# Kernel optimization log

Measured on AMD Instinct MI355X. Metric: run time of the kernel, lower is better.

Reference implementation:

```python
import jax, jax.numpy as jnp
import numpy as np
from jax import lax

B, T_PAST, T_FUT, F_IN, F_OUT, H = 512, 128, 48, 64, 16, 512


def setup_inputs() -> dict:
    key = jax.random.key(0)
    ks = jax.random.split(key, 12)
    s = jnp.float32(0.05)
    p = lambda k, shape: jax.random.normal(k, shape, jnp.float32) * s
    return {
        "inp": jax.random.normal(ks[0], (B, T_PAST, F_IN), jnp.float32),
        "target_seq": jax.random.normal(ks[1], (B, T_FUT, F_OUT), jnp.float32),
        "enc1_Wk": p(ks[2], (F_IN, 4 * H)), "enc1_Wr": p(ks[3], (H, 4 * H)), "enc1_b": jnp.zeros((4 * H,), jnp.float32),
        "enc2_Wk": p(ks[4], (H, 4 * H)), "enc2_Wr": p(ks[5], (H, 4 * H)), "enc2_b": jnp.zeros((4 * H,), jnp.float32),
        "dec1_Wk": p(ks[6], (F_OUT, 4 * H)), "dec1_Wr": p(ks[7], (H, 4 * H)), "dec1_b": jnp.zeros((4 * H,), jnp.float32),
        "dec2_Wk": p(ks[8], (H, 4 * H)), "dec2_Wr": p(ks[9], (H, 4 * H)), "dec2_b": jnp.zeros((4 * H,), jnp.float32),
        "fc_W": p(ks[10], (H, F_OUT)), "fc_b": jnp.zeros((F_OUT,), jnp.float32),
    }


def _gates(z, c_prev):
    # Keras gate order: i, f, g(cell), o
    i, f, g, o = jnp.split(z, 4, axis=-1)
    c = jax.nn.sigmoid(f) * c_prev + jax.nn.sigmoid(i) * jnp.tanh(g)
    h = jax.nn.sigmoid(o) * jnp.tanh(c)
    return h, c


def _lstm_layer(xs, h0, c0, Wk, Wr, b):
    # xs: (B, T, D) -> (hs (B,T,H), hT, cT)
    xz = jnp.einsum("btd,dg->btg", xs, Wk) + b  # input projection precomputed
    def step(carry, xz_t):
        h, c = carry
        h2, c2 = _gates(xz_t + h @ Wr, c)
        return (h2, c2), h2
    (hT, cT), hs = lax.scan(step, (h0, c0), jnp.swapaxes(xz, 0, 1))
    return jnp.swapaxes(hs, 0, 1), hT, cT


def reference(inp, target_seq,
              enc1_Wk, enc1_Wr, enc1_b, enc2_Wk, enc2_Wr, enc2_b,
              dec1_Wk, dec1_Wr, dec1_b, dec2_Wk, dec2_Wr, dec2_b,
              fc_W, fc_b):
    b = inp.shape[0]
    z = jnp.zeros((b, H), inp.dtype)
    # Encoder: layer2 initial state = layer1 final state (as in source)
    h1s, h1, c1 = _lstm_layer(inp, z, z, enc1_Wk, enc1_Wr, enc1_b)
    _, h2, c2 = _lstm_layer(h1s, h1, c1, enc2_Wk, enc2_Wr, enc2_b)
    # Decoder: every future step restarts from (h2, c2) with teacher-forced
    # inputs -> steps are independent, compute all in parallel.
    z1 = (jnp.einsum("btf,fg->btg", target_seq, dec1_Wk)
          + (h2 @ dec1_Wr)[:, None, :] + dec1_b)          # (B, Tf, 4H)
    h1d, c1d = _gates(z1, c2[:, None, :])
    # layer2: input = h1d, initial state = (h1d, c1d) (chained per source)
    z2 = jnp.einsum("bth,hg->btg", h1d, dec2_Wk + dec2_Wr) + dec2_b
    h2d, _ = _gates(z2, c1d)
    return jnp.einsum("bth,hf->btf", h2d, fc_W) + fc_b    # (B, Tf, F_OUT)
```

## Files before the change

kernel.cpp:

```cpp
#include <hip/hip_runtime.h>


typedef _Float16 f16;
typedef _Float16 h8 __attribute__((ext_vector_type(8)));
typedef _Float16 h4 __attribute__((ext_vector_type(4)));
typedef _Float16 h2v __attribute__((ext_vector_type(2)));
typedef float f32x4 __attribute__((ext_vector_type(4)));
typedef float f32x2 __attribute__((ext_vector_type(2)));
typedef unsigned long long ull;

#define DEV static __device__ __forceinline__

constexpr int NB   = 512;
constexpr int TP   = 128;
constexpr int TFU  = 48;
constexpr int FIN  = 64;
constexpr int FOUT = 16;
constexpr int HS   = 512;
constexpr int G4   = 2048;

DEV float sigf(float x) { return 1.0f / (1.0f + __expf(-x)); }
DEV float tanh_(float x) { float e = __expf(2.0f * x); return 1.0f - 2.0f / (e + 1.0f); }

DEV void issue_ld(h8& d, const f16* p) {
  asm volatile("global_load_dwordx4 %0, %1, off" : "=v"(d) : "v"(p));
}
DEV void issue_ldc(h8& d, const f16* p) {
  asm volatile("global_load_dwordx4 %0, %1, off sc0 sc1" : "=v"(d) : "v"(p));
}
#define ASM_VM0    asm volatile("s_waitcnt vmcnt(0)" ::: "memory")
#define ASM_VMC(N) asm volatile("s_waitcnt vmcnt(" #N ")" ::: "memory")
#define SBAR       __builtin_amdgcn_sched_barrier(0)

DEV void st_coh_h2(f16* p, h2v v) {
  union { h2v h; unsigned u; } c;
  c.h = v;
  __hip_atomic_store((unsigned*)p, c.u, __ATOMIC_RELAXED, __HIP_MEMORY_SCOPE_AGENT);
}

DEV unsigned xcc_id() {
  unsigned x;
  asm("s_getreg_b32 %0, hwreg(HW_REG_XCC_ID)" : "=s"(x));
  return x & 7;
}

DEV int ic2zc(int ic) { return ((ic >> 4) & 3) * 512 + ((ic >> 6) << 4) + (ic & 15); }

__global__ void k_conv(const float* __restrict__ a, const float* __restrict__ b,
                       f16* __restrict__ a16, f16* __restrict__ b16) {
  const size_t NA = (size_t)NB * TP * FIN;
  const size_t NBT = (size_t)NB * TFU * FOUT;
  for (size_t i = (size_t)blockIdx.x * blockDim.x + threadIdx.x; i < NA + NBT;
       i += (size_t)gridDim.x * blockDim.x) {
    if (i < NA) a16[i] = (f16)a[i];
    else        b16[i - NA] = (f16)b[i - NA];
  }
}

__global__ void k_bias(const float* __restrict__ b1, const float* __restrict__ b2,
                       const float* __restrict__ b3, const float* __restrict__ b4,
                       float* __restrict__ o1, float* __restrict__ o2,
                       float* __restrict__ o3, float* __restrict__ o4) {
  int ic = blockIdx.x * blockDim.x + threadIdx.x;
  if (ic < G4) {
    int zc = ic2zc(ic);
    o1[ic] = b1[zc]; o2[ic] = b2[zc]; o3[ic] = b3[zc]; o4[ic] = b4[zc];
  }
}

__global__ void k_pack(const float* __restrict__ A, const float* __restrict__ Bs,
                       int split, int NKC, int mode, f16* __restrict__ dst) {
  int i = blockIdx.x * blockDim.x + threadIdx.x;
  int total = 128 * NKC * 64;
  if (i >= total) return;
  int lane = i & 63, rem = i >> 6;
  int kc = rem % NKC, nt = rem / NKC;
  int zc = ic2zc(nt * 16 + (lane & 15));
  int k0 = kc * 32 + ((lane >> 4) << 3);
  h8 v;
#pragma unroll
  for (int j = 0; j < 8; j++) {
    int k = k0 + j;
    float x;
    if (mode == 2) x = A[(size_t)k * G4 + zc] + Bs[(size_t)k * G4 + zc];
    else x = (k < split) ? A[(size_t)k * G4 + zc] : Bs[(size_t)(k - split) * G4 + zc];
    v[j] = (f16)x;
  }
  *(h8*)(dst + (size_t)i * 8) = v;
}

__global__ void k_pack_dk16(const float* __restrict__ W, f16* __restrict__ dst) {
  int i = blockIdx.x * blockDim.x + threadIdx.x;
  if (i >= 128 * 64) return;
  int lane = i & 63, nt = i >> 6;
  int zc = ic2zc(nt * 16 + (lane & 15));
  h4 v;
#pragma unroll
  for (int j = 0; j < 4; j++) v[j] = (f16)W[(size_t)(((lane >> 4) << 2) + j) * G4 + zc];
  *(h4*)(dst + (size_t)i * 4) = v;
}

__global__ void k_pack_fc(const float* __restrict__ W, f16* __restrict__ dst) {
  int i = blockIdx.x * blockDim.x + threadIdx.x;
  if (i >= 32 * 64) return;
  int lane = i & 63, q = i >> 6;
  h4 v;
#pragma unroll
  for (int j = 0; j < 4; j++) {
    int k = q * 16 + ((lane >> 4) << 2) + j;
    v[j] = (f16)W[(size_t)k * FOUT + (lane & 15)];
  }
  *(h4*)(dst + (size_t)i * 4) = v;
}

template <int L, bool HIST>
__global__ __launch_bounds__(512, 2) void k_enc(
    const f16* __restrict__ wfrag, const float* __restrict__ biasI,
    f16* __restrict__ h1s, f16* __restrict__ h2r, f16* __restrict__ h2s,
    float* __restrict__ cT, const float* __restrict__ cInit,
    const f16* __restrict__ inp16, unsigned int* __restrict__ cnt,
    int* __restrict__ roster) {
  constexpr int XKC = (L == 1) ? 2 : 16;
  constexpr int XKH = XKC / 2;
  constexpr int NKC = XKC + 16;
  constexpr size_t SLOT = (size_t)NB * HS;
  constexpr bool PLAIN_H = (L == 1) || HIST;

  extern __shared__ __align__(16) char smem[];
  f16* Bl = (f16*)smem;
  float* zl = (float*)(smem + (size_t)NKC * 4096);
  __shared__ int s_gc[2];

  const int tid = threadIdx.x, lane = tid & 63, wid = tid >> 6;
  const int wr4 = wid & 3, ks = wid >> 2;

  if (tid == 0) {
    unsigned x = xcc_id();
    int slot = atomicAdd(&roster[x], 1) & 31;
    s_gc[0] = (int)x; s_gc[1] = slot;
  }
  __syncthreads();
  const int g = s_gc[0], c = s_gc[1];
  const int b0 = g * 64;
  const int l15 = lane & 15, lk = (lane >> 4) << 3;
  const int trow = tid >> 3, tcol = (tid & 7) << 1;

  const int kc0 = ((c >> 1) + 1) & 15;

  {
    const uint4* src = (const uint4*)wfrag + (size_t)c * NKC * 256;
    uint4* dst = (uint4*)smem;
    for (int i = tid; i < NKC * 256; i += 512) dst[i] = src[i];
  }

  float bs[4][2];
#pragma unroll
  for (int ga = 0; ga < 4; ga++) {
    f32x2 bv = *(const f32x2*)(biasI + 64 * c + 16 * ga + tcol);
    bs[ga][0] = bv[0]; bs[ga][1] = bv[1];
  }

  float cst[2];
  if (L == 1) {
    cst[0] = cst[1] = 0.0f;
  } else {
    f32x2 cv = *(const f32x2*)(cInit + (size_t)(b0 + trow) * HS + 16 * c + tcol);
    cst[0] = cv[0]; cst[1] = cv[1];
  }

  const int arow = b0 + 16 * wr4 + l15;

  const f16* bbase[4];
#pragma unroll
  for (int n = 0; n < 4; n++) bbase[n] = Bl + ((size_t)n * NKC * 64 + lane) * 8;

  const size_t aoff = ((size_t)(lk >> 4) * 512 + arow) * 16 + (lk & 8);

  unsigned int* cbase = cnt + (size_t)g * TP * 16;

  __syncthreads();

  for (int t = 0; t < TP; t++) {
    h8 ax[XKH];
    if (L == 1) {
      const f16* xb = inp16 + ((size_t)arow * TP + t) * FIN + lk + ks * 32;
      issue_ld(ax[0], xb);
    } else {
      const f16* xp = h1s + (size_t)(t + 1) * SLOT + aoff + (size_t)ks * XKH * 16384;
#pragma unroll
      for (int kc = 0; kc < XKH; kc++) {
        issue_ld(ax[kc], xp);
        xp += 16384;
      }
    }
    ASM_VM0; SBAR;

    f32x4 acc[4] = {};
#pragma unroll
    for (int kc = 0; kc < XKH; kc++) {
      int kg = ks * XKH + kc;
#pragma unroll
      for (int n = 0; n < 4; n++) {
        h8 bb = *(const h8*)(bbase[n] + (size_t)kg * 512);
        acc[n] = __builtin_amdgcn_mfma_f32_16x16x32_f16(ax[kc], bb, acc[n], 0, 0, 0);
      }
    }

    if (t > 0) {
      const unsigned int* cp = cbase + (size_t)(t - 1) * 16;
      while (__hip_atomic_load(cp, __ATOMIC_RELAXED, __HIP_MEMORY_SCOPE_AGENT) < 32u)
        __builtin_amdgcn_s_sleep(1);
      SBAR;
    }

    const f16* hb;
    if (L == 1) hb = h1s + (size_t)t * SLOT;
    else if (HIST) hb = (t == 0) ? (h1s + (size_t)TP * SLOT) : (h2s + (size_t)(t - 1) * SLOT);
    else hb = (t == 0) ? (h1s + (size_t)TP * SLOT) : (h2r + (size_t)((t - 1) & 1) * SLOT);
    const f16* hpb = hb + aoff;

    h8 hA[4], hB[4];
#define LD_H(D, P) { if constexpr (PLAIN_H) issue_ld(D, P); else issue_ldc(D, P); }
#define HB_ISSUE4(R, P)                                                        \
  {                                                                            \
    _Pragma("unroll") for (int j = 0; j < 4; j++) {                            \
      int kk = (kc0 + 8 * ks + (P) + j) & 15;                                  \
      const f16* q = hpb + (size_t)kk * 16384;                                 \
      LD_H(R[j], q)                                                            \
    }                                                                          \
  }
#define HB_MFMA4(R, P)                                                         \
  {                                                                            \
    _Pragma("unroll") for (int j = 0; j < 4; j++) {                            \
      int kk = (kc0 + 8 * ks + (P) + j) & 15;                                  \
      _Pragma("unroll") for (int n = 0; n < 4; n++) {                          \
        h8 bb = *(const h8*)(bbase[n] + (size_t)(XKC + kk) * 512);             \
        acc[n] = __builtin_amdgcn_mfma_f32_16x16x32_f16(R[j], bb, acc[n], 0, 0, 0); \
      }                                                                        \
    }                                                                          \
  }

    HB_ISSUE4(hA, 0)
    HB_ISSUE4(hB, 4)
    ASM_VMC(4); SBAR;
    HB_MFMA4(hA, 0)
    ASM_VMC(0); SBAR;
    HB_MFMA4(hB, 4)
#undef HB_ISSUE4
#undef HB_MFMA4
#undef LD_H

    {
      int zr = 16 * wr4 + ((lane >> 4) << 2);
      if (ks == 0) {
#pragma unroll
        for (int n = 0; n < 4; n++) {
          int zc_ = 16 * n + l15;
#pragma unroll
          for (int r = 0; r < 4; r++) zl[(size_t)(zr + r) * 68 + zc_] = acc[n][r];
        }
      }
      __syncthreads();
      if (ks == 1) {
#pragma unroll
        for (int n = 0; n < 4; n++) {
          int zc_ = 16 * n + l15;
#pragma unroll
          for (int r = 0; r < 4; r++) {
            float* p = &zl[(size_t)(zr + r) * 68 + zc_];
            *p += acc[n][r];
          }
        }
      }
      __syncthreads();
    }

    h2v hv;
    {
      const float* zrow = zl + (size_t)trow * 68 + tcol;
      f32x2 z0 = *(const f32x2*)(zrow + 0);
      f32x2 z1 = *(const f32x2*)(zrow + 16);
      f32x2 z2 = *(const f32x2*)(zrow + 32);
      f32x2 z3 = *(const f32x2*)(zrow + 48);
#pragma unroll
      for (int jj = 0; jj < 2; jj++) {
        float zi = z0[jj] + bs[0][jj];
        float zf = z1[jj] + bs[1][jj];
        float zg = z2[jj] + bs[2][jj];
        float zo = z3[jj] + bs[3][jj];
        float ci = sigf(zf) * cst[jj] + sigf(zi) * tanh_(zg);
        cst[jj] = ci;
        hv[jj] = (f16)(sigf(zo) * tanh_(ci));
      }
    }
    {
      f16* hsl;
      if (L == 1) hsl = h1s + (size_t)(t + 1) * SLOT;
      else if (HIST) hsl = h2s + (size_t)t * SLOT;
      else hsl = h2r + (size_t)(t & 1) * SLOT;
      f16* hp = hsl + ((size_t)c * 512 + b0 + trow) * 16 + tcol;
      if constexpr (PLAIN_H) *(h2v*)hp = hv;
      else st_coh_h2(hp, hv);
    }
    if (t == TP - 1) {
      f32x2 cp;
      cp[0] = cst[0]; cp[1] = cst[1];
      *(f32x2*)(cT + (size_t)(b0 + trow) * HS + 16 * c + tcol) = cp;
    }

    ASM_VM0;
    __syncthreads();
    if (tid == 0)
      __hip_atomic_fetch_add(cbase + (size_t)t * 16, 1u, __ATOMIC_RELAXED,
                             __HIP_MEMORY_SCOPE_AGENT);
  }
}

__global__ __launch_bounds__(256) void k_d1(const f16* __restrict__ h2T,
                                            const f16* __restrict__ wF,
                                            const float* __restrict__ bI,
                                            float* __restrict__ u) {
  const int tid = threadIdx.x, lane = tid & 63, wid = tid >> 6;
  const int wr = wid & 1, wc = wid >> 1;
  const int r0 = (blockIdx.x >> 4) * 32, ic0 = (blockIdx.x & 15) * 128;
  const int l15 = lane & 15, lk = (lane >> 4) << 3;
  const int arow = r0 + 16 * wr + l15;
  const f16* abase = h2T + ((size_t)(lk >> 4) * 512 + arow) * 16 + (lk & 8);
  const int nt0 = (ic0 >> 4) + 4 * wc;
  f32x4 acc[4] = {};
#pragma unroll
  for (int kc = 0; kc < 16; kc++) {
    h8 a = *(const h8*)(abase + (size_t)kc * 16384);
#pragma unroll
    for (int n = 0; n < 4; n++) {
      h8 b = *(const h8*)(wF + ((size_t)(nt0 + n) * 16 + kc) * 512 + (size_t)lane * 8);
      acc[n] = __builtin_amdgcn_mfma_f32_16x16x32_f16(a, b, acc[n], 0, 0, 0);
    }
  }
#pragma unroll
  for (int n = 0; n < 4; n++)
#pragma unroll
    for (int r = 0; r < 4; r++) {
      int row = r0 + 16 * wr + ((lane >> 4) << 2) + r;
      int ic = ic0 + 64 * wc + 16 * n + l15;
      u[(size_t)row * G4 + ic] = acc[n][r] + bI[ic];
    }
}

__global__ __launch_bounds__(256, 1) void k_d2(
    const f16* __restrict__ tg16, const f16* __restrict__ wk16F,
    const float* __restrict__ u, const float* __restrict__ c2T,
    const f16* __restrict__ w2F, const float* __restrict__ b2I,
    const f16* __restrict__ fcF, const float* __restrict__ fcb,
    float* __restrict__ out) {
  extern __shared__ __align__(16) char smem[];
  constexpr size_t H1OFF = 0;
  constexpr size_t C1OFF = 65536;
  constexpr size_t H2OFF = 131072;
  constexpr size_t RDOFF = 143360;

  const int tid = threadIdx.x, lane = tid & 63, wid = tid >> 6;
  const int l15 = lane & 15;
  const int r0 = blockIdx.x * 64;

  {
    const int wr = wid & 1, wc = wid >> 1;
    h4 a[2];
#pragma unroll
    for (int m = 0; m < 2; m++)
      a[m] = *(const h4*)(tg16 + (size_t)(r0 + 32 * wr + 16 * m + l15) * FOUT +
                          ((lane >> 4) << 2));
#pragma unroll 1
    for (int hc = 0; hc < 8; hc++) {
      f32x4 acc[2][8] = {};
#pragma unroll
      for (int n = 0; n < 8; n++) {
        int ntg = 16 * hc + 8 * wc + n;
        h4 b = *(const h4*)(wk16F + ((size_t)ntg * 64 + lane) * 4);
        acc[0][n] = __builtin_amdgcn_mfma_f32_16x16x16f16(a[0], b, acc[0][n], 0, 0, 0);
        acc[1][n] = __builtin_amdgcn_mfma_f32_16x16x16f16(a[1], b, acc[1][n], 0, 0, 0);
      }
#pragma unroll
      for (int m = 0; m < 2; m++)
#pragma unroll
        for (int s = 0; s < 2; s++) {
          int qq = 4 * hc + 2 * wc + s;
          int colh = 16 * qq + l15;
          int icb = 256 * hc + 128 * wc + 64 * s + l15;
#pragma unroll
          for (int r = 0; r < 4; r++) {
            int rl = 32 * wr + 16 * m + ((lane >> 4) << 2) + r;
            int grow = r0 + rl;
            int bidx = grow / 48;
            const float* ub = u + (size_t)bidx * G4;
            float zi = acc[m][4 * s + 0][r] + ub[icb];
            float zf = acc[m][4 * s + 1][r] + ub[icb + 16];
            float zg = acc[m][4 * s + 2][r] + ub[icb + 32];
            float zo = acc[m][4 * s + 3][r] + ub[icb + 48];
            float c2v = c2T[(size_t)bidx * HS + colh];
            float c1 = sigf(zf) * c2v + sigf(zi) * tanh_(zg);
            float h1 = sigf(zo) * tanh_(c1);
            size_t hb = (((size_t)rl * 1024) + (size_t)colh * 2) ^ (size_t)((rl & 7) << 4);
            *(f16*)(smem + H1OFF + hb) = (f16)h1;
            *(f16*)(smem + C1OFF + (size_t)rl * 1024 + (size_t)colh * 2) = (f16)c1;
          }
        }
    }
  }
  __syncthreads();

  {
    const int w = wid;
    f32x4 facc[4] = {};
#pragma unroll 1
    for (int sc = 0; sc < 8; sc++) {
      f32x4 acc[4][4] = {};
#pragma unroll
      for (int kc = 0; kc < 16; kc++) {
        h8 a[4];
#pragma unroll
        for (int mt = 0; mt < 4; mt++) {
          int rl = 16 * mt + l15;
          size_t ab = (((size_t)rl * 1024) + (size_t)(kc * 32 + ((lane >> 4) << 3)) * 2) ^
                      (size_t)((rl & 7) << 4);
          a[mt] = *(const h8*)(smem + H1OFF + ab);
        }
#pragma unroll
        for (int n = 0; n < 4; n++) {
          int nt = 32 * w + 4 * sc + n;
          h8 b = *(const h8*)(w2F + ((size_t)nt * 16 + kc) * 512 + (size_t)lane * 8);
#pragma unroll
          for (int mt = 0; mt < 4; mt++)
            acc[mt][n] = __builtin_amdgcn_mfma_f32_16x16x32_f16(a[mt], b, acc[mt][n], 0, 0, 0);
        }
      }
      int qq = 8 * w + sc;
#pragma unroll
      for (int mt = 0; mt < 4; mt++)
#pragma unroll
        for (int r = 0; r < 4; r++) {
          int rl = 16 * mt + ((lane >> 4) << 2) + r;
          int colh = 16 * qq + l15;
          int ic = 512 * w + 64 * sc + l15;
          float zi = acc[mt][0][r] + b2I[ic];
          float zf = acc[mt][1][r] + b2I[ic + 16];
          float zg = acc[mt][2][r] + b2I[ic + 32];
          float zo = acc[mt][3][r] + b2I[ic + 48];
          float c1v = (float)*(const f16*)(smem + C1OFF + (size_t)rl * 1024 + (size_t)colh * 2);
          float cn = sigf(zf) * c1v + sigf(zi) * tanh_(zg);
          float h2v_ = sigf(zo) * tanh_(cn);
          *(f16*)(smem + H2OFF + (size_t)w * 3072 + (size_t)rl * 48 + (size_t)l15 * 2) = (f16)h2v_;
        }
#pragma unroll
      for (int mt = 0; mt < 4; mt++) {
        h4 aa = *(const h4*)(smem + H2OFF + (size_t)w * 3072 + (size_t)(16 * mt + l15) * 48 +
                             ((lane >> 4) << 3));
        h4 bb = *(const h4*)(fcF + ((size_t)qq * 64 + lane) * 4);
        facc[mt] = __builtin_amdgcn_mfma_f32_16x16x16f16(aa, bb, facc[mt], 0, 0, 0);
      }
    }
#pragma unroll
    for (int mt = 0; mt < 4; mt++)
#pragma unroll
      for (int r = 0; r < 4; r++) {
        int rl = 16 * mt + ((lane >> 4) << 2) + r;
        *(float*)(smem + RDOFF + ((size_t)w * 1152 + (size_t)rl * 18 + l15) * 4) = facc[mt][r];
      }
  }
  __syncthreads();

  {
    int rl = tid >> 2, c4 = (tid & 3) * 4;
    f32x4 o;
#pragma unroll
    for (int j = 0; j < 4; j++) {
      float s = 0.0f;
#pragma unroll
      for (int w = 0; w < 4; w++)
        s += *(const float*)(smem + RDOFF + ((size_t)w * 1152 + (size_t)rl * 18 + c4 + j) * 4);
      o[j] = s + fcb[c4 + j];
    }
    *(f32x4*)(out + (size_t)(r0 + rl) * FOUT + c4) = o;
  }
}

extern "C" void kernel_launch(void* const* d_in, const int* in_sizes, int n_in,
                              void* d_out, int out_size, void* d_ws, size_t ws_size,
                              hipStream_t stream) {
  const float* inp     = (const float*)d_in[0];
  const float* target  = (const float*)d_in[1];
  const float* e1Wk    = (const float*)d_in[2];
  const float* e1Wr    = (const float*)d_in[3];
  const float* e1b     = (const float*)d_in[4];
  const float* e2Wk    = (const float*)d_in[5];
  const float* e2Wr    = (const float*)d_in[6];
  const float* e2b     = (const float*)d_in[7];
  const float* d1Wk    = (const float*)d_in[8];
  const float* d1Wr    = (const float*)d_in[9];
  const float* d1b     = (const float*)d_in[10];
  const float* d2Wk    = (const float*)d_in[11];
  const float* d2Wr    = (const float*)d_in[12];
  const float* d2b     = (const float*)d_in[13];
  const float* fcW     = (const float*)d_in[14];
  const float* fcb     = (const float*)d_in[15];
  float* out = (float*)d_out;

  char* ws = (char*)d_ws;
  size_t off = 0;
  auto carve = [&](size_t bytes) { char* p = ws + off; off += bytes; return p; };
  f16*   inp16 = (f16*)carve((size_t)NB * TP * FIN * 2);
  f16*   tg16  = (f16*)carve((size_t)NB * TFU * FOUT * 2);
  f16*   h1s   = (f16*)carve((size_t)(TP + 1) * NB * HS * 2);
  f16*   h2r   = (f16*)carve((size_t)2 * NB * HS * 2);
  float* c1T   = (float*)carve((size_t)NB * HS * 4);
  float* c2T   = (float*)carve((size_t)NB * HS * 4);
  float* ubuf  = (float*)carve((size_t)NB * G4 * 4);
  f16*   Wc1F  = (f16*)carve((size_t)576 * G4 * 2);
  f16*   Wc2F  = (f16*)carve((size_t)1024 * G4 * 2);
  f16*   d1WrF = (f16*)carve((size_t)512 * G4 * 2);
  f16*   W2sF  = (f16*)carve((size_t)512 * G4 * 2);
  f16*   dk16F = (f16*)carve((size_t)16 * G4 * 2);
  f16*   fcWF  = (f16*)carve((size_t)512 * FOUT * 2);
  float* eB1I  = (float*)carve((size_t)G4 * 4);
  float* eB2I  = (float*)carve((size_t)G4 * 4);
  float* dB1I  = (float*)carve((size_t)G4 * 4);
  float* dB2I  = (float*)carve((size_t)G4 * 4);
  unsigned int* cnt1 = (unsigned int*)carve((size_t)8 * TP * 64);
  unsigned int* cnt2 = (unsigned int*)carve((size_t)8 * TP * 64);
  int*   roster = (int*)carve(256);
  const size_t H2S_BYTES = (size_t)TP * NB * HS * 2;
  bool hist = (ws_size >= off + H2S_BYTES);
  f16* h2s = hist ? (f16*)carve(H2S_BYTES) : nullptr;
  (void)n_in; (void)in_sizes; (void)out_size;

  constexpr int LDS_E1 = 18 * 4096 + 64 * 68 * 4;
  constexpr int LDS_E2 = 32 * 4096 + 64 * 68 * 4;
  constexpr int LDS_D2 = 143360 + 18432;
  {
    void (*p1)(const f16*, const float*, f16*, f16*, f16*, float*, const float*, const f16*,
               unsigned int*, int*) = k_enc<1, true>;
    void (*p2a)(const f16*, const float*, f16*, f16*, f16*, float*, const float*, const f16*,
                unsigned int*, int*) = k_enc<2, true>;
    void (*p2b)(const f16*, const float*, f16*, f16*, f16*, float*, const float*, const f16*,
                unsigned int*, int*) = k_enc<2, false>;
    hipFuncSetAttribute((const void*)p1, hipFuncAttributeMaxDynamicSharedMemorySize, LDS_E1);
    hipFuncSetAttribute((const void*)p2a, hipFuncAttributeMaxDynamicSharedMemorySize, LDS_E2);
    hipFuncSetAttribute((const void*)p2b, hipFuncAttributeMaxDynamicSharedMemorySize, LDS_E2);
    hipFuncSetAttribute((const void*)k_d2, hipFuncAttributeMaxDynamicSharedMemorySize, LDS_D2);
  }

  hipMemsetAsync(cnt1, 0, (size_t)2 * 8 * TP * 64 + 256, stream);
  hipMemsetAsync(h1s, 0, (size_t)NB * HS * 2, stream);

  k_conv<<<4096, 256, 0, stream>>>(inp, target, inp16, tg16);
  k_bias<<<8, 256, 0, stream>>>(e1b, e2b, d1b, d2b, eB1I, eB2I, dB1I, dB2I);
  k_pack<<<576, 256, 0, stream>>>(e1Wk, e1Wr, 64, 18, 1, Wc1F);
  k_pack<<<1024, 256, 0, stream>>>(e2Wk, e2Wr, 512, 32, 1, Wc2F);
  k_pack<<<512, 256, 0, stream>>>(d1Wr, d1Wr, 512, 16, 1, d1WrF);
  k_pack<<<512, 256, 0, stream>>>(d2Wk, d2Wr, 0, 16, 2, W2sF);
  k_pack_dk16<<<32, 256, 0, stream>>>(d1Wk, dk16F);
  k_pack_fc<<<8, 256, 0, stream>>>(fcW, fcWF);

  k_enc<1, true><<<256, 512, LDS_E1, stream>>>(Wc1F, eB1I, h1s, h2r, h2s, c1T, nullptr,
                                               inp16, cnt1, roster);
  int* roster2 = roster + 8;
  if (hist)
    k_enc<2, true><<<256, 512, LDS_E2, stream>>>(Wc2F, eB2I, h1s, h2r, h2s, c2T, c1T,
                                                 nullptr, cnt2, roster2);
  else
    k_enc<2, false><<<256, 512, LDS_E2, stream>>>(Wc2F, eB2I, h1s, h2r, h2s, c2T, c1T,
                                                  nullptr, cnt2, roster2);

  const f16* h2T = hist ? (h2s + (size_t)(TP - 1) * NB * HS) : (h2r + (size_t)1 * NB * HS);
  k_d1<<<256, 256, 0, stream>>>(h2T, d1WrF, dB1I, ubuf);
  k_d2<<<384, 256, LDS_D2, stream>>>(tg16, dk16F, ubuf, c2T, W2sF, dB2I, fcWF, fcb, out);
}
```

Measured before the change: 1.291 ms.

## Exchange half-accumulators between K-split waves and defer input MFMA past wait

The LDS reduction of the two K-split partial sums, which took two block barriers and a full z tile round-trip, becomes a single barrier exchange. Each wave writes only the half of its accumulator rows that its partner needs, then finishes gates for its own two rows straight from registers. The input-projection loads are issued before the spin-wait on the previous step's counter, and their MFMAs now run after the hidden-state loads are issued, overlapping the wait and load latency. The cost is narrower global stores of h and c (single f16 or float per lane instead of pairs), including 16-bit coherent atomic stores.

```diff
diff --git a/kernel.cpp b/kernel.cpp
--- a/kernel.cpp
+++ b/kernel.cpp
@@ -32,10 +32,10 @@
 #define ASM_VMC(N) asm volatile("s_waitcnt vmcnt(" #N ")" ::: "memory")
 #define SBAR       __builtin_amdgcn_sched_barrier(0)
 
-DEV void st_coh_h2(f16* p, h2v v) {
-  union { h2v h; unsigned u; } c;
+DEV void st_coh_h1(f16* p, f16 v) {
+  union { f16 h; unsigned short u; } c;
   c.h = v;
-  __hip_atomic_store((unsigned*)p, c.u, __ATOMIC_RELAXED, __HIP_MEMORY_SCOPE_AGENT);
+  __hip_atomic_store((unsigned short*)p, c.u, __ATOMIC_RELAXED, __HIP_MEMORY_SCOPE_AGENT);
 }
 
 DEV unsigned xcc_id() {
@@ -128,7 +128,7 @@
 
   extern __shared__ __align__(16) char smem[];
   f16* Bl = (f16*)smem;
-  float* zl = (float*)(smem + (size_t)NKC * 4096);
+  float* exl = (float*)(smem + (size_t)NKC * 4096);
   __shared__ int s_gc[2];
 
   const int tid = threadIdx.x, lane = tid & 63, wid = tid >> 6;
@@ -143,7 +143,6 @@
   const int g = s_gc[0], c = s_gc[1];
   const int b0 = g * 64;
   const int l15 = lane & 15, lk = (lane >> 4) << 3;
-  const int trow = tid >> 3, tcol = (tid & 7) << 1;
 
   const int kc0 = ((c >> 1) + 1) & 15;
 
@@ -153,19 +152,19 @@
     for (int i = tid; i < NKC * 256; i += 512) dst[i] = src[i];
   }
 
-  float bs[4][2];
-#pragma unroll
-  for (int ga = 0; ga < 4; ga++) {
-    f32x2 bv = *(const f32x2*)(biasI + 64 * c + 16 * ga + tcol);
-    bs[ga][0] = bv[0]; bs[ga][1] = bv[1];
-  }
+  float bv[4];
+#pragma unroll
+  for (int n = 0; n < 4; n++) bv[n] = biasI[64 * c + 16 * n + l15];
+
+  const int grow0 = b0 + 16 * wr4 + ((lane >> 4) << 2) + 2 * ks;
 
   float cst[2];
   if (L == 1) {
     cst[0] = cst[1] = 0.0f;
   } else {
-    f32x2 cv = *(const f32x2*)(cInit + (size_t)(b0 + trow) * HS + 16 * c + tcol);
-    cst[0] = cv[0]; cst[1] = cv[1];
+#pragma unroll
+    for (int j = 0; j < 2; j++)
+      cst[j] = cInit[(size_t)(grow0 + j) * HS + 16 * c + l15];
   }
 
   const int arow = b0 + 16 * wr4 + l15;
@@ -177,6 +176,9 @@
   const size_t aoff = ((size_t)(lk >> 4) * 512 + arow) * 16 + (lk & 8);
 
   unsigned int* cbase = cnt + (size_t)g * TP * 16;
+
+  const int myslot = wr4 * 2 + ks, pslot = wr4 * 2 + (ks ^ 1);
+  const int j2p = 2 * (ks ^ 1);
 
   __syncthreads();
 
@@ -193,24 +195,14 @@
         xp += 16384;
       }
     }
-    ASM_VM0; SBAR;
-
-    f32x4 acc[4] = {};
-#pragma unroll
-    for (int kc = 0; kc < XKH; kc++) {
-      int kg = ks * XKH + kc;
-#pragma unroll
-      for (int n = 0; n < 4; n++) {
-        h8 bb = *(const h8*)(bbase[n] + (size_t)kg * 512);
-        acc[n] = __builtin_amdgcn_mfma_f32_16x16x32_f16(ax[kc], bb, acc[n], 0, 0, 0);
-      }
-    }
 
     if (t > 0) {
       const unsigned int* cp = cbase + (size_t)(t - 1) * 16;
       while (__hip_atomic_load(cp, __ATOMIC_RELAXED, __HIP_MEMORY_SCOPE_AGENT) < 32u)
         __builtin_amdgcn_s_sleep(1);
       SBAR;
+    } else {
+      ASM_VM0; SBAR;
     }
 
     const f16* hb;
@@ -242,6 +234,19 @@
 
     HB_ISSUE4(hA, 0)
     HB_ISSUE4(hB, 4)
+
+    f32x4 acc[4] = {};
+
+#pragma unroll
+    for (int kc = 0; kc < XKH; kc++) {
+      int kg = ks * XKH + kc;
+#pragma unroll
+      for (int n = 0; n < 4; n++) {
+        h8 bb = *(const h8*)(bbase[n] + (size_t)kg * 512);
+        acc[n] = __builtin_amdgcn_mfma_f32_16x16x32_f16(ax[kc], bb, acc[n], 0, 0, 0);
+      }
+    }
+
     ASM_VMC(4); SBAR;
     HB_MFMA4(hA, 0)
     ASM_VMC(0); SBAR;
@@ -250,62 +255,40 @@
 #undef HB_MFMA4
 #undef LD_H
 
-    {
-      int zr = 16 * wr4 + ((lane >> 4) << 2);
-      if (ks == 0) {
-#pragma unroll
-        for (int n = 0; n < 4; n++) {
-          int zc_ = 16 * n + l15;
-#pragma unroll
-          for (int r = 0; r < 4; r++) zl[(size_t)(zr + r) * 68 + zc_] = acc[n][r];
-        }
-      }
-      __syncthreads();
-      if (ks == 1) {
-#pragma unroll
-        for (int n = 0; n < 4; n++) {
-          int zc_ = 16 * n + l15;
-#pragma unroll
-          for (int r = 0; r < 4; r++) {
-            float* p = &zl[(size_t)(zr + r) * 68 + zc_];
-            *p += acc[n][r];
-          }
-        }
-      }
-      __syncthreads();
-    }
-
-    h2v hv;
-    {
-      const float* zrow = zl + (size_t)trow * 68 + tcol;
-      f32x2 z0 = *(const f32x2*)(zrow + 0);
-      f32x2 z1 = *(const f32x2*)(zrow + 16);
-      f32x2 z2 = *(const f32x2*)(zrow + 32);
-      f32x2 z3 = *(const f32x2*)(zrow + 48);
-#pragma unroll
-      for (int jj = 0; jj < 2; jj++) {
-        float zi = z0[jj] + bs[0][jj];
-        float zf = z1[jj] + bs[1][jj];
-        float zg = z2[jj] + bs[2][jj];
-        float zo = z3[jj] + bs[3][jj];
-        float ci = sigf(zf) * cst[jj] + sigf(zi) * tanh_(zg);
-        cst[jj] = ci;
-        hv[jj] = (f16)(sigf(zo) * tanh_(ci));
-      }
+#pragma unroll
+    for (int n = 0; n < 4; n++)
+#pragma unroll
+      for (int j = 0; j < 2; j++)
+        exl[(size_t)myslot * 512 + (size_t)(n * 2 + j) * 64 + lane] = acc[n][j2p + j];
+    __syncthreads();
+
+    f16 hval[2];
+#pragma unroll
+    for (int j = 0; j < 2; j++) {
+      float zi = acc[0][2 * ks + j] + exl[(size_t)pslot * 512 + (size_t)(0 + j) * 64 + lane] + bv[0];
+      float zf = acc[1][2 * ks + j] + exl[(size_t)pslot * 512 + (size_t)(2 + j) * 64 + lane] + bv[1];
+      float zg = acc[2][2 * ks + j] + exl[(size_t)pslot * 512 + (size_t)(4 + j) * 64 + lane] + bv[2];
+      float zo = acc[3][2 * ks + j] + exl[(size_t)pslot * 512 + (size_t)(6 + j) * 64 + lane] + bv[3];
+      float ci = sigf(zf) * cst[j] + sigf(zi) * tanh_(zg);
+      cst[j] = ci;
+      hval[j] = (f16)(sigf(zo) * tanh_(ci));
     }
     {
       f16* hsl;
       if (L == 1) hsl = h1s + (size_t)(t + 1) * SLOT;
       else if (HIST) hsl = h2s + (size_t)t * SLOT;
       else hsl = h2r + (size_t)(t & 1) * SLOT;
-      f16* hp = hsl + ((size_t)c * 512 + b0 + trow) * 16 + tcol;
-      if constexpr (PLAIN_H) *(h2v*)hp = hv;
-      else st_coh_h2(hp, hv);
+#pragma unroll
+      for (int j = 0; j < 2; j++) {
+        f16* hp = hsl + ((size_t)c * 512 + grow0 + j) * 16 + l15;
+        if constexpr (PLAIN_H) *hp = hval[j];
+        else st_coh_h1(hp, hval[j]);
+      }
     }
     if (t == TP - 1) {
-      f32x2 cp;
-      cp[0] = cst[0]; cp[1] = cst[1];
-      *(f32x2*)(cT + (size_t)(b0 + trow) * HS + 16 * c + tcol) = cp;
+#pragma unroll
+      for (int j = 0; j < 2; j++)
+        cT[(size_t)(grow0 + j) * HS + 16 * c + l15] = cst[j];
     }
 
     ASM_VM0;
```

Result: slower. 1.666 ms (+29.0%).
